# Performance work log

Hardware: AMD Instinct MI355X
Metric: run time of the kernel (lower is better)

The kernel has to match this reference:

```python
import jax, jax.numpy as jnp
import numpy as np

B, N, DIM = 2, 2048, 4096
N_HEAD, N_KV_HEAD = 32, 8
HEAD_DIM = DIM // N_HEAD  # 128
N_REP = N_HEAD // N_KV_HEAD  # 4


def _rope_cos_sin(n, half_dim, theta=500000.0):
    inv = 1.0 / (theta ** (np.arange(0, half_dim, dtype=np.float64) / half_dim))
    ang = np.arange(n, dtype=np.float64)[:, None] * inv[None, :]
    return jnp.asarray(np.cos(ang), jnp.float32), jnp.asarray(np.sin(ang), jnp.float32)


def setup_inputs() -> dict:
    key = jax.random.key(0)
    ks = jax.random.split(key, 5)
    s = 0.02
    x = jax.random.normal(ks[0], (B, N, DIM), jnp.float32)
    wq = jax.random.normal(ks[1], (DIM, DIM), jnp.float32) * s
    wk = jax.random.normal(ks[2], (N_KV_HEAD * HEAD_DIM, DIM), jnp.float32) * s
    wv = jax.random.normal(ks[3], (N_KV_HEAD * HEAD_DIM, DIM), jnp.float32) * s
    wo = jax.random.normal(ks[4], (DIM, DIM), jnp.float32) * s
    cos, sin = _rope_cos_sin(N, HEAD_DIM // 2)
    # additive causal mask [N, N]
    mask = jnp.where(jnp.tril(jnp.ones((N, N), bool)), 0.0, -1e9).astype(jnp.float32)
    return {"x": x, "wq": wq, "wk": wk, "wv": wv, "wo": wo,
            "cos": cos, "sin": sin, "mask": mask, "start_pos": 0}


def apply_rope(x, cos, sin):
    # x: [b, n, h, d]; rotate consecutive pairs (complex mult)
    b, n, h, d = x.shape
    xr = x.reshape(b, n, h, d // 2, 2)
    x0, x1 = xr[..., 0], xr[..., 1]
    c = cos[None, :, None, :]
    s = sin[None, :, None, :]
    o0 = x0 * c - x1 * s
    o1 = x0 * s + x1 * c
    return jnp.stack([o0, o1], axis=-1).reshape(b, n, h, d)


def reference(x, wq, wk, wv, wo, cos, sin, mask, start_pos):
    b, n, _ = x.shape
    q = (x @ wq.T).reshape(b, n, N_HEAD, HEAD_DIM)
    k = (x @ wk.T).reshape(b, n, N_KV_HEAD, HEAD_DIM)
    v = (x @ wv.T).reshape(b, n, N_KV_HEAD, HEAD_DIM)
    q = apply_rope(q, cos, sin)
    k = apply_rope(k, cos, sin)
    # GQA: group query heads over kv heads (avoids materializing repeated k/v)
    qg = q.reshape(b, n, N_KV_HEAD, N_REP, HEAD_DIM)
    scale = 1.0 / jnp.sqrt(jnp.float32(HEAD_DIM))
    scores = jnp.einsum('bqhrd,bkhd->bhrqk', qg, k) * scale
    scores = scores + mask[None, None, None, :, :]
    probs = jax.nn.softmax(scores.astype(jnp.float32), axis=-1).astype(q.dtype)
    out = jnp.einsum('bhrqk,bkhd->bqhrd', probs, v)
    out = out.reshape(b, n, N_HEAD * HEAD_DIM)
    return out @ wo.T
```

## Files before the change

### kernel.cpp

```cpp
#include <hip/hip_runtime.h>
#include <hip/hip_bf16.h>
#include <stdint.h>

#define BB 2
#define NN 2048
#define DIM 4096
#define NH 32
#define NKV 8
#define HD 128

typedef __attribute__((ext_vector_type(8))) short short8;
typedef __attribute__((ext_vector_type(4))) float floatx4;
typedef __attribute__((ext_vector_type(16))) float floatx16;

__device__ __forceinline__ float bf2f(uint16_t u) {
  union { uint32_t u; float f; } c; c.u = ((uint32_t)u) << 16; return c.f;
}
__device__ __forceinline__ uint16_t f2bf(float f) {
  union { float f; uint32_t u; } c; c.f = f;
  uint32_t u = c.u;
  return (uint16_t)((u + 0x7fffu + ((u >> 16) & 1u)) >> 16);
}

typedef const __attribute__((address_space(1))) uint32_t* gas_t;
typedef __attribute__((address_space(3))) uint32_t* las_t;
__device__ __forceinline__ void gl2lds16(const uint16_t* g, uint16_t* l) {
  __builtin_amdgcn_global_load_lds((gas_t)(uintptr_t)g,
                                   (las_t)(uint32_t)(uintptr_t)l, 16, 0, 0);
}

__global__ void cvt_bf16(const float* __restrict__ in, uint16_t* __restrict__ out,
                         long n4) {
  long i = (long)blockIdx.x * 256 + threadIdx.x;
  if (i >= n4) return;
  float4 v = ((const float4*)in)[i];
  uint16_t t[4] = {f2bf(v.x), f2bf(v.y), f2bf(v.z), f2bf(v.w)};
  ((uint64_t*)out)[i] = *(uint64_t*)t;
}

template <bool CF32>
__global__ __launch_bounds__(512, 2) void gemm256_k(const uint16_t* __restrict__ A,
                                                    const uint16_t* __restrict__ B,
                                                    void* __restrict__ Cv,
                                                    int N, int K, int NX) {
  extern __shared__ __align__(16) uint16_t lds2[];
  const int tid = threadIdx.x;
  const int wave = tid >> 6, lane = tid & 63;
  const int quad = lane >> 4, l16 = lane & 15;
  const int wm = wave >> 2, wn = wave & 3;
  const int NT = K >> 6;
  const int cswz = (l16 & 7) << 4;

  const int nwg = gridDim.x;
  const int q8 = nwg >> 3, r8 = nwg & 7, xc = blockIdx.x & 7, sq = blockIdx.x >> 3;
  const int lin = (xc < r8 ? xc * (q8 + 1) : r8 * (q8 + 1) + (xc - r8) * q8) + sq;
  const int m0 = (lin / NX) * 256, n0 = (lin % NX) * 256;

  const int srow = tid >> 3;
  const int scolB = ((tid & 7) * 16) ^ ((srow & 7) << 4);

#define STAGEU(tt, opB_, h_)                                                        \
  {                                                                                 \
    const uint16_t* gsrc = (opB_) ? B : A;                                          \
    const int rb = (opB_) ? n0 : m0;                                                \
    char* lb = (char*)lds2 + ((tt) & 1) * 65536 + (opB_) * 32768 + (h_) * 16384;    \
    _Pragma("unroll")                                                               \
    for (int pp = 0; pp < 2; ++pp) {                                                \
      int rr = (h_) * 128 + pp * 64 + srow;                                         \
      const char* g = (const char*)(gsrc + (size_t)(rb + rr) * K + (tt) * 64) + scolB; \
      gl2lds16((const uint16_t*)g, (uint16_t*)(lb + pp * 8192 + tid * 16));         \
    }                                                                               \
  }

#define LDA8(kk_)                                                                   \
  _Pragma("unroll")                                                                 \
  for (int m_ = 0; m_ < 8; ++m_) {                                                  \
    int rA = wm * 128 + m_ * 16 + l16;                                              \
    a[m_][kk_] = *(const short8*)(bufA + rA * 128 +                                 \
                                  (((kk_) * 64 + quad * 16) ^ cswz));               \
  }
#define LDB4(kk_)                                                                   \
  _Pragma("unroll")                                                                 \
  for (int n_ = 0; n_ < 4; ++n_) {                                                  \
    int rB = wn * 64 + n_ * 16 + l16;                                               \
    b[n_][kk_] = *(const short8*)(bufB + rB * 128 +                                 \
                                  (((kk_) * 64 + quad * 16) ^ cswz));               \
  }

#define MMCLUSTER(kk_, nlo_)                                                        \
  _Pragma("unroll")                                                                 \
  for (int m_ = 0; m_ < 8; ++m_) {                                                  \
    acc[m_][nlo_] = __builtin_amdgcn_mfma_f32_16x16x32_bf16(a[m_][kk_], b[nlo_][kk_], acc[m_][nlo_], 0, 0, 0); \
    acc[m_][nlo_ + 1] = __builtin_amdgcn_mfma_f32_16x16x32_bf16(a[m_][kk_], b[(nlo_) + 1][kk_], acc[m_][(nlo_) + 1], 0, 0, 0); \
  }

#define SYNC_PRE()                                           \
  do {                                                       \
    __builtin_amdgcn_s_barrier();                            \
    asm volatile("s_waitcnt lgkmcnt(0)" ::: "memory");       \
    __builtin_amdgcn_sched_barrier(0);                       \
    __builtin_amdgcn_s_setprio(1);                           \
  } while (0)
#define SYNC_POST()                                          \
  do {                                                       \
    __builtin_amdgcn_s_setprio(0);                           \
    __builtin_amdgcn_s_barrier();                            \
  } while (0)

  short8 a[8][2], b[4][2];
  floatx4 acc[8][4] = {};

  STAGEU(0, 0, 0);
  STAGEU(0, 1, 0);
  STAGEU(0, 0, 1);
  STAGEU(0, 1, 1);
  if (NT > 1) {
    STAGEU(1, 0, 0);
    STAGEU(1, 1, 0);
    asm volatile("s_waitcnt vmcnt(4)" ::: "memory");
  } else {
    asm volatile("s_waitcnt vmcnt(0)" ::: "memory");
  }
  __builtin_amdgcn_s_barrier();

  for (int t = 0; t < NT; ++t) {
    const char* bufA = (const char*)lds2 + (t & 1) * 65536;
    const char* bufB = bufA + 32768;
    LDA8(0);
    LDB4(0);
    if (t + 1 < NT) STAGEU(t + 1, 0, 1);
    SYNC_PRE();
    MMCLUSTER(0, 0);
    SYNC_POST();
    LDA8(1);
    LDB4(1);
    if (t + 1 < NT) STAGEU(t + 1, 1, 1);
    SYNC_PRE();
    MMCLUSTER(0, 2);
    SYNC_POST();
    if (t + 2 < NT) STAGEU(t + 2, 0, 0);
    SYNC_PRE();
    MMCLUSTER(1, 0);
    SYNC_POST();
    if (t + 2 < NT) STAGEU(t + 2, 1, 0);
    __builtin_amdgcn_s_barrier();
    asm volatile("s_waitcnt lgkmcnt(0)" ::: "memory");
    __builtin_amdgcn_sched_barrier(0);
    __builtin_amdgcn_s_setprio(1);
    MMCLUSTER(1, 2);
    __builtin_amdgcn_s_setprio(0);
    if (t + 2 < NT)
      asm volatile("s_waitcnt vmcnt(4)" ::: "memory");
    else
      asm volatile("s_waitcnt vmcnt(0)" ::: "memory");
    __builtin_amdgcn_s_barrier();
  }

#pragma unroll
  for (int m_ = 0; m_ < 8; ++m_) {
#pragma unroll
    for (int r = 0; r < 4; ++r) {
      int row = m0 + wm * 128 + m_ * 16 + quad * 4 + r;
#pragma unroll
      for (int n_ = 0; n_ < 4; ++n_) {
        int col = n0 + wn * 64 + n_ * 16 + l16;
        if constexpr (CF32)
          ((float*)Cv)[(size_t)row * N + col] = acc[m_][n_][r];
        else
          ((uint16_t*)Cv)[(size_t)row * N + col] = f2bf(acc[m_][n_][r]);
      }
    }
  }
#undef STAGEU
#undef LDA8
#undef LDB4
#undef MMCLUSTER
#undef SYNC_PRE
#undef SYNC_POST
}

template <bool CF32>
__device__ __forceinline__ void gemm_core(const uint16_t* __restrict__ A,
                                          const uint16_t* __restrict__ B,
                                          void* __restrict__ Cv,
                                          int N, int K, int m0, int n0,
                                          uint16_t* As, uint16_t* Bs) {
  const int tid = threadIdx.x;
  const int wave = tid >> 6, lane = tid & 63;
  const int quad = lane >> 4, l16 = lane & 15;
  const int wm = (wave >> 1) * 64, wn = (wave & 1) * 64;

  const int srow = wave * 32 + (lane >> 2);
  const int scol = (lane & 3) * 8;
  const uint16_t* gA = A + (size_t)(m0 + srow) * K + scol;
  const uint16_t* gB = B + (size_t)(n0 + srow) * K + scol;
  uint16_t* lA = &As[wave * 1024 + lane * 8];
  uint16_t* lB = &Bs[wave * 1024 + lane * 8];

  floatx4 acc[4][4] = {};

  for (int kb = 0; kb < K; kb += 32) {
    gl2lds16(gA + kb, lA);
    gl2lds16(gA + kb + (size_t)16 * K, lA + 16 * 32);
    gl2lds16(gB + kb, lB);
    gl2lds16(gB + kb + (size_t)16 * K, lB + 16 * 32);
    __syncthreads();

    short8 a[4], b[4];
#pragma unroll
    for (int i = 0; i < 4; ++i)
      a[i] = *(const short8*)(&As[(wm + i * 16 + l16) * 32 + quad * 8]);
#pragma unroll
    for (int j = 0; j < 4; ++j)
      b[j] = *(const short8*)(&Bs[(wn + j * 16 + l16) * 32 + quad * 8]);
#pragma unroll
    for (int i = 0; i < 4; ++i)
#pragma unroll
      for (int j = 0; j < 4; ++j)
        acc[i][j] = __builtin_amdgcn_mfma_f32_16x16x32_bf16(a[i], b[j], acc[i][j], 0, 0, 0);
    __syncthreads();
  }

#pragma unroll
  for (int i = 0; i < 4; ++i)
#pragma unroll
    for (int r = 0; r < 4; ++r) {
      int row = m0 + wm + i * 16 + quad * 4 + r;
#pragma unroll
      for (int j = 0; j < 4; ++j) {
        int col = n0 + wn + j * 16 + l16;
        if constexpr (CF32)
          ((float*)Cv)[(size_t)row * N + col] = acc[i][j][r];
        else
          ((uint16_t*)Cv)[(size_t)row * N + col] = f2bf(acc[i][j][r]);
      }
    }
}

template <bool CF32>
__global__ __launch_bounds__(256) void gemm_fast(const uint16_t* __restrict__ A,
                                                 const uint16_t* __restrict__ B,
                                                 void* __restrict__ Cv,
                                                 int N, int K) {
  __shared__ __align__(16) uint16_t As[128 * 32];
  __shared__ __align__(16) uint16_t Bs[128 * 32];
  gemm_core<CF32>(A, B, Cv, N, K, blockIdx.y * 128, blockIdx.x * 128, As, Bs);
}

__global__ __launch_bounds__(256) void gemm_kv2(const uint16_t* __restrict__ A,
                                                const uint16_t* __restrict__ WK,
                                                const uint16_t* __restrict__ WV,
                                                uint16_t* __restrict__ KO,
                                                uint16_t* __restrict__ VTO) {
  __shared__ __align__(16) uint16_t As[128 * 32];
  __shared__ __align__(16) uint16_t Bs[128 * 32];
  if (blockIdx.z == 0)
    gemm_core<false>(A, WK, KO, 1024, DIM, blockIdx.y * 128, blockIdx.x * 128, As, Bs);
  else
    gemm_core<false>(WV, A, VTO, 4096, DIM, blockIdx.x * 128, blockIdx.y * 128, As, Bs);
}

template <bool F32>
__device__ __forceinline__ void load8(const void* __restrict__ base, size_t off,
                                      uint16_t* __restrict__ lds) {
  if constexpr (F32) {
    const float* p = (const float*)base + off;
    float4 a = *(const float4*)p;
    float4 b = *(const float4*)(p + 4);
    uint16_t t[8];
    t[0] = f2bf(a.x); t[1] = f2bf(a.y); t[2] = f2bf(a.z); t[3] = f2bf(a.w);
    t[4] = f2bf(b.x); t[5] = f2bf(b.y); t[6] = f2bf(b.z); t[7] = f2bf(b.w);
    *(float4*)lds = *(float4*)t;
  } else {
    *(float4*)lds = *(const float4*)((const uint16_t*)base + off);
  }
}

template <bool AF32, bool BF32, bool CF32>
__global__ __launch_bounds__(256) void gemm_bt(const void* __restrict__ Av,
                                               const void* __restrict__ Bv,
                                               void* __restrict__ Cv,
                                               int M, int N, int K) {
  __shared__ __align__(16) uint16_t As[128 * 32];
  __shared__ __align__(16) uint16_t Bs[128 * 32];
  const int tid = threadIdx.x;
  const int wave = tid >> 6, lane = tid & 63;
  const int quad = lane >> 4, l16 = lane & 15;
  const int m0 = blockIdx.y * 128, n0 = blockIdx.x * 128;
  const int wm = (wave >> 1) * 64, wn = (wave & 1) * 64;

  floatx4 acc[4][4] = {};

  for (int kb = 0; kb < K; kb += 32) {
    int s = tid;
#pragma unroll
    for (int i = 0; i < 2; ++i, s += 256) {
      int row = s >> 2, cs = (s & 3) * 8;
      load8<AF32>(Av, (size_t)(m0 + row) * K + kb + cs, &As[row * 32 + cs]);
      load8<BF32>(Bv, (size_t)(n0 + row) * K + kb + cs, &Bs[row * 32 + cs]);
    }
    __syncthreads();

    short8 a[4], b[4];
#pragma unroll
    for (int i = 0; i < 4; ++i)
      a[i] = *(const short8*)(&As[(wm + i * 16 + l16) * 32 + quad * 8]);
#pragma unroll
    for (int j = 0; j < 4; ++j)
      b[j] = *(const short8*)(&Bs[(wn + j * 16 + l16) * 32 + quad * 8]);
#pragma unroll
    for (int i = 0; i < 4; ++i)
#pragma unroll
      for (int j = 0; j < 4; ++j)
        acc[i][j] = __builtin_amdgcn_mfma_f32_16x16x32_bf16(a[i], b[j], acc[i][j], 0, 0, 0);
    __syncthreads();
  }

#pragma unroll
  for (int i = 0; i < 4; ++i)
#pragma unroll
    for (int r = 0; r < 4; ++r) {
      int row = m0 + wm + i * 16 + quad * 4 + r;
#pragma unroll
      for (int j = 0; j < 4; ++j) {
        int col = n0 + wn + j * 16 + l16;
        if constexpr (CF32)
          ((float*)Cv)[(size_t)row * N + col] = acc[i][j][r];
        else
          ((uint16_t*)Cv)[(size_t)row * N + col] = f2bf(acc[i][j][r]);
      }
    }
}

__global__ void rope_kernel(uint16_t* __restrict__ qk,
                            const float* __restrict__ cosb,
                            const float* __restrict__ sinb, int H, int total,
                            float scale) {
  int idx = blockIdx.x * blockDim.x + threadIdx.x;
  if (idx >= total) return;
  int p = idx & 63;
  int nh = idx >> 6;
  int bn = nh / H;
  int n = bn & (NN - 1);
  size_t base = (size_t)nh * 128 + p * 2;
  uint32_t pr = *(const uint32_t*)(&qk[base]);
  float x0 = bf2f((uint16_t)(pr & 0xffff));
  float x1 = bf2f((uint16_t)(pr >> 16));
  float c = cosb[n * 64 + p];
  float s = sinb[n * 64 + p];
  float o0 = (x0 * c - x1 * s) * scale;
  float o1 = (x0 * s + x1 * c) * scale;
  *(uint32_t*)(&qk[base]) = (uint32_t)f2bf(o0) | ((uint32_t)f2bf(o1) << 16);
}

#define KSTR 136
#define VSTR 72
#define PSTR 72

__global__ __launch_bounds__(256, 2) void flash_attn(const uint16_t* __restrict__ Q,
                                                     const uint16_t* __restrict__ K,
                                                     const uint16_t* __restrict__ V,
                                                     uint16_t* __restrict__ O) {
  __shared__ __align__(16) uint16_t Ks[64 * KSTR];
  __shared__ __align__(16) uint16_t Vt[128 * VSTR];
  __shared__ __align__(16) uint16_t Ps[4][32 * PSTR];

  const int tid = threadIdx.x;
  const int wave = tid >> 6, lane = tid & 63;
  const int quad = lane >> 4, l16 = lane & 15;
  const int b = blockIdx.z, h = blockIdx.y, kvh = h >> 2;
  const int qt = gridDim.x - 1 - blockIdx.x;
  const int qlo = qt * 128 + wave * 32;

  short8 aq[2][4];
#pragma unroll
  for (int mi = 0; mi < 2; ++mi) {
    const uint16_t* qrow = Q + (((size_t)(b * NN + qlo + mi * 16 + l16)) * NH + h) * HD;
#pragma unroll
    for (int kd = 0; kd < 4; ++kd)
      aq[mi][kd] = *(const short8*)(&qrow[kd * 32 + quad * 8]);
  }

  float mr[2][4], lr[2][4];
  floatx4 accO[2][8] = {};
#pragma unroll
  for (int mi = 0; mi < 2; ++mi)
#pragma unroll
    for (int r = 0; r < 4; ++r) { mr[mi][r] = -1e30f; lr[mi][r] = 0.f; }

  const float sc2 = 0.08838834764831845f * 1.4426950408889634f;
  const int ntiles = 2 * qt + 2;

  const int srow = tid >> 4;
  const int sl16 = tid & 15;
  const int d8 = sl16 * 8;

  for (int t = 0; t < ntiles; ++t) {
    const int kv0 = t * 64;

#pragma unroll
    for (int i = 0; i < 4; ++i) {
      int row = srow + i * 16;
      size_t gb = (((size_t)(b * NN + kv0 + row)) * NKV + kvh) * HD + d8;
      *(float4*)(&Ks[row * KSTR + d8]) = *(const float4*)(&K[gb]);
      uint16_t vv[8];
      *(float4*)vv = *(const float4*)(&V[gb]);
      int kvp = row ^ ((sl16 & 7) << 3);
#pragma unroll
      for (int j = 0; j < 8; ++j) Vt[(d8 + j) * VSTR + kvp] = vv[j];
    }
    __syncthreads();

    if (kv0 <= qlo + 31) {
      floatx4 s[2][4] = {};
#pragma unroll
      for (int jn = 0; jn < 4; ++jn)
#pragma unroll
        for (int kd = 0; kd < 4; ++kd) {
          short8 bk = *(const short8*)(&Ks[(jn * 16 + l16) * KSTR + kd * 32 + quad * 8]);
          s[0][jn] = __builtin_amdgcn_mfma_f32_16x16x32_bf16(aq[0][kd], bk, s[0][jn], 0, 0, 0);
          s[1][jn] = __builtin_amdgcn_mfma_f32_16x16x32_bf16(aq[1][kd], bk, s[1][jn], 0, 0, 0);
        }

      const bool needmask = (kv0 + 63) > qlo;
#pragma unroll
      for (int mi = 0; mi < 2; ++mi)
#pragma unroll
        for (int jn = 0; jn < 4; ++jn)
#pragma unroll
          for (int r = 0; r < 4; ++r) {
            float v = s[mi][jn][r] * sc2;
            if (needmask) {
              int qr = qlo + mi * 16 + quad * 4 + r;
              int kc = kv0 + jn * 16 + l16;
              if (kc > qr) v = -1e30f;
            }
            s[mi][jn][r] = v;
          }

#pragma unroll
      for (int mi = 0; mi < 2; ++mi)
#pragma unroll
        for (int r = 0; r < 4; ++r) {
          float mx = fmaxf(fmaxf(s[mi][0][r], s[mi][1][r]), fmaxf(s[mi][2][r], s[mi][3][r]));
#pragma unroll
          for (int off = 1; off < 16; off <<= 1)
            mx = fmaxf(mx, __shfl_xor(mx, off, 64));
          float mn = fmaxf(mr[mi][r], mx);
          float al = exp2f(mr[mi][r] - mn);
          mr[mi][r] = mn;
          float rs = 0.f;
#pragma unroll
          for (int jn = 0; jn < 4; ++jn) {
            float p = exp2f(s[mi][jn][r] - mn);
            s[mi][jn][r] = p;
            rs += p;
          }
#pragma unroll
          for (int off = 1; off < 16; off <<= 1)
            rs += __shfl_xor(rs, off, 64);
          lr[mi][r] = lr[mi][r] * al + rs;
#pragma unroll
          for (int jn = 0; jn < 4; ++jn)
            Ps[wave][(mi * 16 + quad * 4 + r) * PSTR + jn * 16 + l16] = f2bf(s[mi][jn][r]);
#pragma unroll
          for (int dt = 0; dt < 8; ++dt) accO[mi][dt][r] *= al;
        }

      short8 ap[2][2];
#pragma unroll
      for (int mi = 0; mi < 2; ++mi)
#pragma unroll
        for (int kk = 0; kk < 2; ++kk)
          ap[mi][kk] = *(const short8*)(&Ps[wave][(mi * 16 + l16) * PSTR + kk * 32 + quad * 8]);
#pragma unroll
      for (int dt = 0; dt < 8; ++dt) {
        int x = (2 * dt + (l16 >> 3)) & 7;
#pragma unroll
        for (int kk = 0; kk < 2; ++kk) {
          int kvb = (kk * 32 + quad * 8) ^ (x << 3);
          short8 bv = *(const short8*)(&Vt[(dt * 16 + l16) * VSTR + kvb]);
          accO[0][dt] = __builtin_amdgcn_mfma_f32_16x16x32_bf16(ap[0][kk], bv, accO[0][dt], 0, 0, 0);
          accO[1][dt] = __builtin_amdgcn_mfma_f32_16x16x32_bf16(ap[1][kk], bv, accO[1][dt], 0, 0, 0);
        }
      }
    }
    __syncthreads();
  }

#pragma unroll
  for (int mi = 0; mi < 2; ++mi)
#pragma unroll
    for (int r = 0; r < 4; ++r) lr[mi][r] = 1.f / lr[mi][r];
#pragma unroll
  for (int mi = 0; mi < 2; ++mi)
#pragma unroll
    for (int dt = 0; dt < 8; ++dt)
#pragma unroll
      for (int r = 0; r < 4; ++r) {
        int qr = qlo + mi * 16 + quad * 4 + r;
        size_t oidx = (((size_t)(b * NN + qr)) * NH + h) * HD + dt * 16 + l16;
        O[oidx] = f2bf(accO[mi][dt][r] * lr[mi][r]);
      }
}

__global__ __launch_bounds__(512, 2) void flash_attn2(const uint16_t* __restrict__ Qb,
                                                      const uint16_t* __restrict__ Kb,
                                                      const uint16_t* __restrict__ VTb,
                                                      uint16_t* __restrict__ Ob) {
  __shared__ __align__(16) uint16_t lds[32768];

  const int tid = threadIdx.x;
  const int wave = tid >> 6, lane = tid & 63;
  const int l31 = lane & 31, hi = lane >> 5;
  const int b = blockIdx.z, h = blockIdx.y, kvh = h >> 2;
  const int qt = gridDim.x - 1 - blockIdx.x;
  const int qbase = qt * 256 + wave * 32;
  const int q_abs = qbase + l31;

  short8 qf[8];
  {
    const uint16_t* qrow = Qb + (((size_t)(b * NN + q_abs)) * NH + h) * HD;
#pragma unroll
    for (int kb = 0; kb < 8; ++kb)
      qf[kb] = *(const short8*)(qrow + kb * 16 + hi * 8);
  }

  floatx16 accO[4] = {};
  float mrow = -1e30f, lrow = 0.f;

  const int ntiles = 4 * qt + 4;

  const int krow = tid >> 4;
  const int kcol = (tid & 15) * 16;
  const int vrow = tid >> 3;
  const int vcol = (tid & 7) * 16;

#define STAGE(T, BUF)                                                               \
  {                                                                                 \
    const int kv0s = (T) * 64;                                                      \
    uint16_t* lb = &lds[(BUF) * 16384];                                             \
    _Pragma("unroll")                                                               \
    for (int p = 0; p < 2; ++p) {                                                   \
      int row = krow + 32 * p;                                                      \
      const char* g = (const char*)(Kb + (((size_t)(b * NN + kv0s + row)) * NKV + kvh) * HD); \
      gl2lds16((const uint16_t*)(g + (kcol ^ ((row & 7) << 4))),                    \
               &lb[tid * 8 + p * 4096]);                                            \
    }                                                                               \
    _Pragma("unroll")                                                               \
    for (int p = 0; p < 2; ++p) {                                                   \
      int d = vrow + 64 * p;                                                        \
      const char* g = (const char*)(VTb + ((size_t)(kvh * 128 + d)) * (BB * NN) +   \
                                    (size_t)b * NN + kv0s);                         \
      gl2lds16((const uint16_t*)(g + (vcol ^ ((d & 7) << 4))),                      \
               &lb[8192 + tid * 8 + p * 4096]);                                     \
    }                                                                               \
  }

  STAGE(0, 0);
  __syncthreads();

  for (int t = 0; t < ntiles; ++t) {
    const int buf = t & 1;
    if (t + 1 < ntiles) STAGE(t + 1, buf ^ 1);

    if (t * 64 <= qbase + 31) {
      const int kv0 = t * 64;
      const uint16_t* Ksb = &lds[buf * 16384];
      const uint16_t* Vsb = &lds[buf * 16384 + 8192];
      const int kswz = (l31 & 7) << 4;

      floatx16 s0 = {}, s1 = {};
      __builtin_amdgcn_s_setprio(1);
#pragma unroll
      for (int kb = 0; kb < 8; ++kb) {
        int colB = (32 * kb + 16 * hi) ^ kswz;
        short8 a0 = *(const short8*)((const char*)Ksb + l31 * 256 + colB);
        short8 a1 = *(const short8*)((const char*)Ksb + l31 * 256 + 8192 + colB);
        s0 = __builtin_amdgcn_mfma_f32_32x32x16_bf16(a0, qf[kb], s0, 0, 0, 0);
        s1 = __builtin_amdgcn_mfma_f32_32x32x16_bf16(a1, qf[kb], s1, 0, 0, 0);
      }
      __builtin_amdgcn_s_setprio(0);

      if (kv0 + 63 > qbase) {
#pragma unroll
        for (int r = 0; r < 16; ++r) {
          int kvl = kv0 + (r & 3) + 8 * (r >> 2) + 4 * hi;
          if (kvl > q_abs) s0[r] = -1e30f;
          if (kvl + 32 > q_abs) s1[r] = -1e30f;
        }
      }

      float pm = fmaxf(s0[0], s1[0]);
#pragma unroll
      for (int r = 1; r < 16; ++r) pm = fmaxf(pm, fmaxf(s0[r], s1[r]));
      pm = fmaxf(pm, __shfl_xor(pm, 32, 64));

      if (!__all(pm - mrow <= 8.f)) {
        float mn = fmaxf(mrow, pm);
        float al = exp2f(mrow - mn);
        mrow = mn;
        lrow *= al;
#pragma unroll
        for (int j = 0; j < 4; ++j)
#pragma unroll
          for (int r = 0; r < 16; ++r) accO[j][r] *= al;
      }

      float rs = 0.f;
#pragma unroll
      for (int r = 0; r < 16; ++r) { float p = exp2f(s0[r] - mrow); s0[r] = p; rs += p; }
#pragma unroll
      for (int r = 0; r < 16; ++r) { float p = exp2f(s1[r] - mrow); s1[r] = p; rs += p; }
      rs += __shfl_xor(rs, 32, 64);
      lrow += rs;

      uint32_t W0[8], W1[8], X0[8], X1[8];
#pragma unroll
      for (int i = 0; i < 8; ++i) {
        W0[i] = (uint32_t)f2bf(s0[2 * i]) | ((uint32_t)f2bf(s0[2 * i + 1]) << 16);
        W1[i] = (uint32_t)f2bf(s1[2 * i]) | ((uint32_t)f2bf(s1[2 * i + 1]) << 16);
      }
#pragma unroll
      for (int i = 0; i < 8; ++i) {
        X0[i] = (uint32_t)__shfl_xor((int)W0[i], 32, 64);
        X1[i] = (uint32_t)__shfl_xor((int)W1[i], 32, 64);
      }

      __builtin_amdgcn_s_setprio(1);
#pragma unroll
      for (int t16 = 0; t16 < 4; ++t16) {
        const uint32_t* Wc = (t16 < 2) ? W0 : W1;
        const uint32_t* Xc = (t16 < 2) ? X0 : X1;
        const int q4 = (t16 & 1) * 4;
        union { uint32_t u[4]; short8 v; } fr;
        fr.u[0] = hi ? Xc[q4 + 2] : Wc[q4 + 0];
        fr.u[1] = hi ? Xc[q4 + 3] : Wc[q4 + 1];
        fr.u[2] = hi ? Wc[q4 + 2] : Xc[q4 + 0];
        fr.u[3] = hi ? Wc[q4 + 3] : Xc[q4 + 1];
        short8 pb = fr.v;
        const int colB = 32 * t16 + 16 * hi;
#pragma unroll
        for (int j = 0; j < 4; ++j) {
          int row = 32 * j + l31;
          short8 av = *(const short8*)((const char*)Vsb + row * 128 + (colB ^ ((row & 7) << 4)));
          accO[j] = __builtin_amdgcn_mfma_f32_32x32x16_bf16(av, pb, accO[j], 0, 0, 0);
        }
      }
      __builtin_amdgcn_s_setprio(0);
    }
    __syncthreads();
  }

  float inv = 1.f / lrow;
  uint16_t* ow = &lds[wave * 4096];
#pragma unroll
  for (int j = 0; j < 4; ++j)
#pragma unroll
    for (int p = 0; p < 8; ++p) {
      int dd = 32 * j + ((2 * p) & 3) + 8 * (p >> 1) + 4 * hi;
      uint32_t w = (uint32_t)f2bf(accO[j][2 * p] * inv) |
                   ((uint32_t)f2bf(accO[j][2 * p + 1] * inv) << 16);
      *(uint32_t*)((char*)ow + l31 * 256 + ((dd * 2) ^ ((l31 & 7) << 4))) = w;
    }
#pragma unroll
  for (int it = 0; it < 8; ++it) {
    int q = it * 4 + (lane >> 4);
    int colB = ((lane & 15) * 16) ^ ((q & 7) << 4);
    short8 v = *(const short8*)((const char*)ow + q * 256 + colB);
    int orow = qt * 256 + wave * 32 + q;
    *(short8*)(Ob + (((size_t)(b * NN + orow)) * NH + h) * HD + (lane & 15) * 8) = v;
  }
#undef STAGE
}

extern "C" void kernel_launch(void* const* d_in, const int* in_sizes, int n_in,
                              void* d_out, int out_size, void* d_ws, size_t ws_size,
                              hipStream_t stream) {
  const float* x    = (const float*)d_in[0];
  const float* wq   = (const float*)d_in[1];
  const float* wk   = (const float*)d_in[2];
  const float* wv   = (const float*)d_in[3];
  const float* wo   = (const float*)d_in[4];
  const float* cosb = (const float*)d_in[5];
  const float* sinb = (const float*)d_in[6];
  float* out = (float*)d_out;

  const size_t M = (size_t)BB * NN;
  const size_t SZ_Q = M * DIM;
  const size_t SZ_W = (size_t)DIM * DIM;
  const size_t SZ_KV = M * NKV * HD;
  const size_t SZ_WKV = (size_t)NKV * HD * DIM;

  const float ATT_SCALE = 0.08838834764831845f * 1.4426950408889634f;

  dim3 blk(256);
  const size_t need_fast =
      2 * (SZ_Q + 3 * SZ_W + 2 * SZ_WKV + 2 * SZ_KV + SZ_Q);

  static int g_dyn_ok = -1;
  if (g_dyn_ok < 0) {
    hipError_t e1 = hipFuncSetAttribute(
        reinterpret_cast<const void*>(&gemm256_k<false>),
        hipFuncAttributeMaxDynamicSharedMemorySize, 131072);
    hipError_t e2 = hipFuncSetAttribute(
        reinterpret_cast<const void*>(&gemm256_k<true>),
        hipFuncAttributeMaxDynamicSharedMemorySize, 131072);
    g_dyn_ok = (e1 == hipSuccess && e2 == hipSuccess) ? 1 : 0;
  }

  if (ws_size >= need_fast) {
    uint16_t* p = (uint16_t*)d_ws;
    uint16_t* xb    = p; p += SZ_Q;
    uint16_t* wqb   = p; p += SZ_W;
    uint16_t* wob   = p; p += SZ_W;
    uint16_t* wkb   = p; p += SZ_WKV;
    uint16_t* wvb   = p; p += SZ_WKV;
    uint16_t* qbuf  = p; p += SZ_Q;
    uint16_t* kbuf  = p; p += SZ_KV;
    uint16_t* vtbuf = p; p += SZ_KV;
    uint16_t* obuf  = p;

    cvt_bf16<<<(int)(SZ_Q / 4 / 256), blk, 0, stream>>>(x, xb, SZ_Q / 4);
    cvt_bf16<<<(int)(SZ_W / 4 / 256), blk, 0, stream>>>(wq, wqb, SZ_W / 4);
    cvt_bf16<<<(int)(SZ_WKV / 4 / 256), blk, 0, stream>>>(wk, wkb, SZ_WKV / 4);
    cvt_bf16<<<(int)(SZ_WKV / 4 / 256), blk, 0, stream>>>(wv, wvb, SZ_WKV / 4);
    cvt_bf16<<<(int)(SZ_W / 4 / 256), blk, 0, stream>>>(wo, wob, SZ_W / 4);

    if (g_dyn_ok)
      gemm256_k<false><<<dim3(256), dim3(512), 131072, stream>>>(xb, wqb, qbuf, DIM, DIM, 16);
    else
      gemm_fast<false><<<dim3(DIM / 128, M / 128), blk, 0, stream>>>(xb, wqb, qbuf, DIM, DIM);

    gemm_kv2<<<dim3(8, 32, 2), blk, 0, stream>>>(xb, wkb, wvb, kbuf, vtbuf);

    int totq = (int)(M * NH * 64);
    int totk = (int)(M * NKV * 64);
    rope_kernel<<<(totq + 255) / 256, blk, 0, stream>>>(qbuf, cosb, sinb, NH, totq, ATT_SCALE);
    rope_kernel<<<(totk + 255) / 256, blk, 0, stream>>>(kbuf, cosb, sinb, NKV, totk, 1.0f);

    flash_attn2<<<dim3(NN / 256, NH, BB), dim3(512), 0, stream>>>(qbuf, kbuf, vtbuf, obuf);

    if (g_dyn_ok)
      gemm256_k<true><<<dim3(256), dim3(512), 131072, stream>>>(obuf, wob, out, DIM, DIM, 16);
    else
      gemm_fast<true><<<dim3(DIM / 128, M / 128), blk, 0, stream>>>(obuf, wob, out, DIM, DIM);
  } else {
    uint16_t* qbuf = (uint16_t*)d_ws;
    uint16_t* kbuf = qbuf + SZ_Q;
    uint16_t* vbuf = kbuf + SZ_KV;
    uint16_t* obuf = vbuf + SZ_KV;

    gemm_bt<true, true, false><<<dim3(DIM / 128, M / 128), blk, 0, stream>>>(x, wq, qbuf, M, DIM, DIM);
    gemm_bt<true, true, false><<<dim3((NKV * HD) / 128, M / 128), blk, 0, stream>>>(x, wk, kbuf, M, NKV * HD, DIM);
    gemm_bt<true, true, false><<<dim3((NKV * HD) / 128, M / 128), blk, 0, stream>>>(x, wv, vbuf, M, NKV * HD, DIM);

    int totq = (int)(M * NH * 64);
    int totk = (int)(M * NKV * 64);
    rope_kernel<<<(totq + 255) / 256, blk, 0, stream>>>(qbuf, cosb, sinb, NH, totq, 1.0f);
    rope_kernel<<<(totk + 255) / 256, blk, 0, stream>>>(kbuf, cosb, sinb, NKV, totk, 1.0f);

    flash_attn<<<dim3(NN / 128, NH, BB), blk, 0, stream>>>(qbuf, kbuf, vbuf, obuf);

    gemm_bt<false, true, true><<<dim3(DIM / 128, M / 128), blk, 0, stream>>>(obuf, wo, out, M, DIM, DIM);
  }
}
```

Before: 792.1 us.

## Use 256-tile GEMM for K/V projections and restructure flash attention scheduling

Factors the 256x256 GEMM body into a reusable core and adds a K/V projection kernel built on it, replacing the older 128-tile K/V GEMM. Flash attention now runs on a 1D grid whose block index is remapped so that blocks sharing a KV head are grouped, which is meant to improve L2 reuse of K/V. It also switches to a wider 16-row LDS swizzle with pointer-increment staging, tree reductions for row max and sum, packed bf16 conversion instructions, and v_permlane32_swap in place of cross-half shuffles. These changes span several independent ideas and carry correctness risk in the new index and swizzle math.

After: 764.6 us. 1.04x faster.

```diff
diff --git a/kernel.cpp b/kernel.cpp
--- a/kernel.cpp
+++ b/kernel.cpp
@@ -39,22 +39,17 @@
 }
 
 template <bool CF32>
-__global__ __launch_bounds__(512, 2) void gemm256_k(const uint16_t* __restrict__ A,
-                                                    const uint16_t* __restrict__ B,
-                                                    void* __restrict__ Cv,
-                                                    int N, int K, int NX) {
-  extern __shared__ __align__(16) uint16_t lds2[];
+__device__ __forceinline__ void g256_core(const uint16_t* __restrict__ A,
+                                          const uint16_t* __restrict__ B,
+                                          void* __restrict__ Cv,
+                                          int N, int K, int m0, int n0,
+                                          uint16_t* lds2) {
   const int tid = threadIdx.x;
   const int wave = tid >> 6, lane = tid & 63;
   const int quad = lane >> 4, l16 = lane & 15;
   const int wm = wave >> 2, wn = wave & 3;
   const int NT = K >> 6;
   const int cswz = (l16 & 7) << 4;
-
-  const int nwg = gridDim.x;
-  const int q8 = nwg >> 3, r8 = nwg & 7, xc = blockIdx.x & 7, sq = blockIdx.x >> 3;
-  const int lin = (xc < r8 ? xc * (q8 + 1) : r8 * (q8 + 1) + (xc - r8) * q8) + sq;
-  const int m0 = (lin / NX) * 256, n0 = (lin % NX) * 256;
 
   const int srow = tid >> 3;
   const int scolB = ((tid & 7) * 16) ^ ((srow & 7) << 4);
@@ -180,6 +175,36 @@
 }
 
 template <bool CF32>
+__global__ __launch_bounds__(512, 2) void gemm256_k(const uint16_t* __restrict__ A,
+                                                    const uint16_t* __restrict__ B,
+                                                    void* __restrict__ Cv,
+                                                    int N, int K, int NX) {
+  extern __shared__ __align__(16) uint16_t lds2[];
+  const int nwg = gridDim.x;
+  const int q8 = nwg >> 3, r8 = nwg & 7, xc = blockIdx.x & 7, sq = blockIdx.x >> 3;
+  const int lin = (xc < r8 ? xc * (q8 + 1) : r8 * (q8 + 1) + (xc - r8) * q8) + sq;
+  const int m0 = (lin / NX) * 256, n0 = (lin % NX) * 256;
+  g256_core<CF32>(A, B, Cv, N, K, m0, n0, lds2);
+}
+
+__global__ __launch_bounds__(512, 2) void gemm_kv256(const uint16_t* __restrict__ xb,
+                                                     const uint16_t* __restrict__ wkb,
+                                                     const uint16_t* __restrict__ wvb,
+                                                     uint16_t* __restrict__ kbuf,
+                                                     uint16_t* __restrict__ vtbuf) {
+  extern __shared__ __align__(16) uint16_t lds2[];
+  const int id = blockIdx.x;
+  if (id < 64) {
+    const int mt = id >> 2, nt = id & 3;
+    g256_core<false>(xb, wkb, kbuf, NKV * HD, DIM, mt * 256, nt * 256, lds2);
+  } else {
+    const int i2 = id - 64;
+    const int mt = i2 & 3, nt = i2 >> 2;
+    g256_core<false>(wvb, xb, vtbuf, BB * NN, DIM, mt * 256, nt * 256, lds2);
+  }
+}
+
+template <bool CF32>
 __device__ __forceinline__ void gemm_core(const uint16_t* __restrict__ A,
                                           const uint16_t* __restrict__ B,
                                           void* __restrict__ Cv,
@@ -245,19 +270,6 @@
   __shared__ __align__(16) uint16_t As[128 * 32];
   __shared__ __align__(16) uint16_t Bs[128 * 32];
   gemm_core<CF32>(A, B, Cv, N, K, blockIdx.y * 128, blockIdx.x * 128, As, Bs);
-}
-
-__global__ __launch_bounds__(256) void gemm_kv2(const uint16_t* __restrict__ A,
-                                                const uint16_t* __restrict__ WK,
-                                                const uint16_t* __restrict__ WV,
-                                                uint16_t* __restrict__ KO,
-                                                uint16_t* __restrict__ VTO) {
-  __shared__ __align__(16) uint16_t As[128 * 32];
-  __shared__ __align__(16) uint16_t Bs[128 * 32];
-  if (blockIdx.z == 0)
-    gemm_core<false>(A, WK, KO, 1024, DIM, blockIdx.y * 128, blockIdx.x * 128, As, Bs);
-  else
-    gemm_core<false>(WV, A, VTO, 4096, DIM, blockIdx.x * 128, blockIdx.y * 128, As, Bs);
 }
 
 template <bool F32>
@@ -513,8 +525,15 @@
   const int tid = threadIdx.x;
   const int wave = tid >> 6, lane = tid & 63;
   const int l31 = lane & 31, hi = lane >> 5;
-  const int b = blockIdx.z, h = blockIdx.y, kvh = h >> 2;
-  const int qt = gridDim.x - 1 - blockIdx.x;
+
+  const int X = blockIdx.x;
+  const int slot = X >> 3;
+  const int g = (X & 7) + ((slot >> 5) << 3);
+  const int w = slot & 31;
+  const int b = g >> 3, kvh = g & 7;
+  const int h = kvh * 4 + (w >> 3);
+  const int qt = 7 - (w & 7);
+
   const int qbase = qt * 256 + wave * 32;
   const int q_abs = qbase + l31;
 
@@ -528,55 +547,50 @@
 
   floatx16 accO[4] = {};
   float mrow = -1e30f, lrow = 0.f;
-
   const int ntiles = 4 * qt + 4;
 
-  const int krow = tid >> 4;
-  const int kcol = (tid & 15) * 16;
-  const int vrow = tid >> 3;
-  const int vcol = (tid & 7) * 16;
-
-#define STAGE(T, BUF)                                                               \
-  {                                                                                 \
-    const int kv0s = (T) * 64;                                                      \
-    uint16_t* lb = &lds[(BUF) * 16384];                                             \
-    _Pragma("unroll")                                                               \
-    for (int p = 0; p < 2; ++p) {                                                   \
-      int row = krow + 32 * p;                                                      \
-      const char* g = (const char*)(Kb + (((size_t)(b * NN + kv0s + row)) * NKV + kvh) * HD); \
-      gl2lds16((const uint16_t*)(g + (kcol ^ ((row & 7) << 4))),                    \
-               &lb[tid * 8 + p * 4096]);                                            \
-    }                                                                               \
-    _Pragma("unroll")                                                               \
-    for (int p = 0; p < 2; ++p) {                                                   \
-      int d = vrow + 64 * p;                                                        \
-      const char* g = (const char*)(VTb + ((size_t)(kvh * 128 + d)) * (BB * NN) +   \
-                                    (size_t)b * NN + kv0s);                         \
-      gl2lds16((const uint16_t*)(g + (vcol ^ ((d & 7) << 4))),                      \
-               &lb[8192 + tid * 8 + p * 4096]);                                     \
-    }                                                                               \
-  }
-
-  STAGE(0, 0);
+  const int toff = (tid & 15) * 16;
+  const int r16 = tid >> 4;
+  const int sswz = (r16 & 15) << 4;
+  const char* gk = (const char*)Kb +
+      (((size_t)(b * NN) + r16) * NKV + kvh) * HD * 2 + (toff ^ sswz);
+  const int vu = toff ^ sswz;
+  const int vd = r16 + ((vu >> 7) << 6);
+  const char* gv = (const char*)VTb +
+      ((size_t)(kvh * 128 + vd)) * (BB * NN) * 2 + (size_t)(b * NN) * 2 + (vu & 127);
+
+#define STAGE(BUF)                                                              \
+  {                                                                             \
+    char* lb = (char*)lds + (BUF) * 32768;                                      \
+    gl2lds16((const uint16_t*)gk, (uint16_t*)(lb + tid * 16));                  \
+    gl2lds16((const uint16_t*)(gk + 65536), (uint16_t*)(lb + 8192 + tid * 16)); \
+    gl2lds16((const uint16_t*)gv, (uint16_t*)(lb + 16384 + tid * 16));          \
+    gl2lds16((const uint16_t*)(gv + 262144),                                    \
+             (uint16_t*)(lb + 24576 + tid * 16));                               \
+    gk += 131072;                                                               \
+    gv += 128;                                                                  \
+  }
+
+  STAGE(0);
   __syncthreads();
 
   for (int t = 0; t < ntiles; ++t) {
     const int buf = t & 1;
-    if (t + 1 < ntiles) STAGE(t + 1, buf ^ 1);
+    if (t + 1 < ntiles) STAGE(buf ^ 1);
 
     if (t * 64 <= qbase + 31) {
       const int kv0 = t * 64;
-      const uint16_t* Ksb = &lds[buf * 16384];
-      const uint16_t* Vsb = &lds[buf * 16384 + 8192];
-      const int kswz = (l31 & 7) << 4;
+      const char* Ksb = (const char*)lds + buf * 32768;
+      const char* Vsb = Ksb + 16384;
+      const int kswz = (l31 & 15) << 4;
 
       floatx16 s0 = {}, s1 = {};
       __builtin_amdgcn_s_setprio(1);
 #pragma unroll
       for (int kb = 0; kb < 8; ++kb) {
-        int colB = (32 * kb + 16 * hi) ^ kswz;
-        short8 a0 = *(const short8*)((const char*)Ksb + l31 * 256 + colB);
-        short8 a1 = *(const short8*)((const char*)Ksb + l31 * 256 + 8192 + colB);
+        int colB = (kb * 32 + hi * 16) ^ kswz;
+        short8 a0 = *(const short8*)(Ksb + l31 * 256 + colB);
+        short8 a1 = *(const short8*)(Ksb + 8192 + l31 * 256 + colB);
         s0 = __builtin_amdgcn_mfma_f32_32x32x16_bf16(a0, qf[kb], s0, 0, 0, 0);
         s1 = __builtin_amdgcn_mfma_f32_32x32x16_bf16(a1, qf[kb], s1, 0, 0, 0);
       }
@@ -591,10 +605,15 @@
         }
       }
 
-      float pm = fmaxf(s0[0], s1[0]);
-#pragma unroll
-      for (int r = 1; r < 16; ++r) pm = fmaxf(pm, fmaxf(s0[r], s1[r]));
-      pm = fmaxf(pm, __shfl_xor(pm, 32, 64));
+      float mx[8];
+#pragma unroll
+      for (int i = 0; i < 8; ++i)
+        mx[i] = fmaxf(fmaxf(s0[i], s0[i + 8]), fmaxf(s1[i], s1[i + 8]));
+#pragma unroll
+      for (int st = 4; st > 0; st >>= 1)
+#pragma unroll
+        for (int i = 0; i < st; ++i) mx[i] = fmaxf(mx[i], mx[i + st]);
+      float pm = fmaxf(mx[0], __shfl_xor(mx[0], 32, 64));
 
       if (!__all(pm - mrow <= 8.f)) {
         float mn = fmaxf(mrow, pm);
@@ -607,43 +626,44 @@
           for (int r = 0; r < 16; ++r) accO[j][r] *= al;
       }
 
-      float rs = 0.f;
-#pragma unroll
-      for (int r = 0; r < 16; ++r) { float p = exp2f(s0[r] - mrow); s0[r] = p; rs += p; }
-#pragma unroll
-      for (int r = 0; r < 16; ++r) { float p = exp2f(s1[r] - mrow); s1[r] = p; rs += p; }
-      rs += __shfl_xor(rs, 32, 64);
-      lrow += rs;
-
-      uint32_t W0[8], W1[8], X0[8], X1[8];
+#pragma unroll
+      for (int r = 0; r < 16; ++r) s0[r] = exp2f(s0[r] - mrow);
+#pragma unroll
+      for (int r = 0; r < 16; ++r) s1[r] = exp2f(s1[r] - mrow);
+      float sm[8];
+#pragma unroll
+      for (int i = 0; i < 8; ++i)
+        sm[i] = (s0[i] + s0[i + 8]) + (s1[i] + s1[i + 8]);
+#pragma unroll
+      for (int st = 4; st > 0; st >>= 1)
+#pragma unroll
+        for (int i = 0; i < st; ++i) sm[i] += sm[i + st];
+      lrow += sm[0] + __shfl_xor(sm[0], 32, 64);
+
+      uint32_t W[16];
 #pragma unroll
       for (int i = 0; i < 8; ++i) {
-        W0[i] = (uint32_t)f2bf(s0[2 * i]) | ((uint32_t)f2bf(s0[2 * i + 1]) << 16);
-        W1[i] = (uint32_t)f2bf(s1[2 * i]) | ((uint32_t)f2bf(s1[2 * i + 1]) << 16);
-      }
-#pragma unroll
-      for (int i = 0; i < 8; ++i) {
-        X0[i] = (uint32_t)__shfl_xor((int)W0[i], 32, 64);
-        X1[i] = (uint32_t)__shfl_xor((int)W1[i], 32, 64);
+        asm("v_cvt_pk_bf16_f32 %0, %1, %2" : "=v"(W[i]) : "v"(s0[2 * i]), "v"(s0[2 * i + 1]));
+        asm("v_cvt_pk_bf16_f32 %0, %1, %2" : "=v"(W[8 + i]) : "v"(s1[2 * i]), "v"(s1[2 * i + 1]));
       }
 
       __builtin_amdgcn_s_setprio(1);
 #pragma unroll
-      for (int t16 = 0; t16 < 4; ++t16) {
-        const uint32_t* Wc = (t16 < 2) ? W0 : W1;
-        const uint32_t* Xc = (t16 < 2) ? X0 : X1;
-        const int q4 = (t16 & 1) * 4;
+      for (int g16 = 0; g16 < 4; ++g16) {
+        const int base = (g16 >> 1) * 8 + (g16 & 1) * 4;
+        uint32_t pa0 = W[base], pb0 = W[base + 2];
+        uint32_t pa1 = W[base + 1], pb1 = W[base + 3];
+        asm volatile("v_permlane32_swap_b32 %0, %1" : "+v"(pa0), "+v"(pb0));
+        asm volatile("v_permlane32_swap_b32 %0, %1" : "+v"(pa1), "+v"(pb1));
         union { uint32_t u[4]; short8 v; } fr;
-        fr.u[0] = hi ? Xc[q4 + 2] : Wc[q4 + 0];
-        fr.u[1] = hi ? Xc[q4 + 3] : Wc[q4 + 1];
-        fr.u[2] = hi ? Wc[q4 + 2] : Xc[q4 + 0];
-        fr.u[3] = hi ? Wc[q4 + 3] : Xc[q4 + 1];
+        fr.u[0] = pa0; fr.u[1] = pa1; fr.u[2] = pb0; fr.u[3] = pb1;
         short8 pb = fr.v;
-        const int colB = 32 * t16 + 16 * hi;
+        const int cb = 32 * g16 + 16 * hi;
 #pragma unroll
         for (int j = 0; j < 4; ++j) {
-          int row = 32 * j + l31;
-          short8 av = *(const short8*)((const char*)Vsb + row * 128 + (colB ^ ((row & 7) << 4)));
+          const int sr = 32 * (j & 1) + l31;
+          short8 av = *(const short8*)(Vsb + sr * 256 +
+                                       (((j >> 1) * 128 + cb) ^ kswz));
           accO[j] = __builtin_amdgcn_mfma_f32_32x32x16_bf16(av, pb, accO[j], 0, 0, 0);
         }
       }
@@ -659,9 +679,9 @@
 #pragma unroll
     for (int p = 0; p < 8; ++p) {
       int dd = 32 * j + ((2 * p) & 3) + 8 * (p >> 1) + 4 * hi;
-      uint32_t w = (uint32_t)f2bf(accO[j][2 * p] * inv) |
-                   ((uint32_t)f2bf(accO[j][2 * p + 1] * inv) << 16);
-      *(uint32_t*)((char*)ow + l31 * 256 + ((dd * 2) ^ ((l31 & 7) << 4))) = w;
+      uint32_t wv = (uint32_t)f2bf(accO[j][2 * p] * inv) |
+                    ((uint32_t)f2bf(accO[j][2 * p + 1] * inv) << 16);
+      *(uint32_t*)((char*)ow + l31 * 256 + ((dd * 2) ^ ((l31 & 7) << 4))) = wv;
     }
 #pragma unroll
   for (int it = 0; it < 8; ++it) {
@@ -706,7 +726,10 @@
     hipError_t e2 = hipFuncSetAttribute(
         reinterpret_cast<const void*>(&gemm256_k<true>),
         hipFuncAttributeMaxDynamicSharedMemorySize, 131072);
-    g_dyn_ok = (e1 == hipSuccess && e2 == hipSuccess) ? 1 : 0;
+    hipError_t e3 = hipFuncSetAttribute(
+        reinterpret_cast<const void*>(&gemm_kv256),
+        hipFuncAttributeMaxDynamicSharedMemorySize, 131072);
+    g_dyn_ok = (e1 == hipSuccess && e2 == hipSuccess && e3 == hipSuccess) ? 1 : 0;
   }
 
   if (ws_size >= need_fast) {
@@ -727,19 +750,21 @@
     cvt_bf16<<<(int)(SZ_WKV / 4 / 256), blk, 0, stream>>>(wv, wvb, SZ_WKV / 4);
     cvt_bf16<<<(int)(SZ_W / 4 / 256), blk, 0, stream>>>(wo, wob, SZ_W / 4);
 
-    if (g_dyn_ok)
+    if (g_dyn_ok) {
       gemm256_k<false><<<dim3(256), dim3(512), 131072, stream>>>(xb, wqb, qbuf, DIM, DIM, 16);
-    else
+      gemm_kv256<<<dim3(128), dim3(512), 131072, stream>>>(xb, wkb, wvb, kbuf, vtbuf);
+    } else {
       gemm_fast<false><<<dim3(DIM / 128, M / 128), blk, 0, stream>>>(xb, wqb, qbuf, DIM, DIM);
-
-    gemm_kv2<<<dim3(8, 32, 2), blk, 0, stream>>>(xb, wkb, wvb, kbuf, vtbuf);
+      gemm_fast<false><<<dim3((NKV * HD) / 128, M / 128), blk, 0, stream>>>(xb, wkb, kbuf, NKV * HD, DIM);
+      gemm_fast<false><<<dim3((int)(M / 128), (NKV * HD) / 128), blk, 0, stream>>>(wvb, xb, vtbuf, (int)M, DIM);
+    }
 
     int totq = (int)(M * NH * 64);
     int totk = (int)(M * NKV * 64);
     rope_kernel<<<(totq + 255) / 256, blk, 0, stream>>>(qbuf, cosb, sinb, NH, totq, ATT_SCALE);
     rope_kernel<<<(totk + 255) / 256, blk, 0, stream>>>(kbuf, cosb, sinb, NKV, totk, 1.0f);
 
-    flash_attn2<<<dim3(NN / 256, NH, BB), dim3(512), 0, stream>>>(qbuf, kbuf, vtbuf, obuf);
+    flash_attn2<<<dim3(512), dim3(512), 0, stream>>>(qbuf, kbuf, vtbuf, obuf);
 
     if (g_dyn_ok)
       gemm256_k<true><<<dim3(256), dim3(512), 131072, stream>>>(obuf, wob, out, DIM, DIM, 16);
```
